# Performance work log

Measured on AMD Instinct MI355X. Metric: run time of the kernel, lower is better.

The kernel has to match this reference:

```python
import jax, jax.numpy as jnp
import numpy as np

N_NODES = 100000


def gcn_conv(x, W, b, src, dst, n_nodes):
    """PyG GCNConv: add self-loops, symmetric normalization, linear, scatter-add, bias."""
    xw = x @ W  # [N, out]
    loop = jnp.arange(n_nodes, dtype=src.dtype)
    src2 = jnp.concatenate([src, loop])  # sources (x_j gathered from here)
    dst2 = jnp.concatenate([dst, loop])  # targets (aggregation index)
    # degree (incl. self-loops) computed at target nodes, unit edge weights
    deg = jax.ops.segment_sum(jnp.ones_like(dst2, dtype=xw.dtype), dst2, num_segments=n_nodes)
    dinv = jnp.where(deg > 0, jax.lax.rsqrt(deg), 0.0)
    norm = dinv[src2] * dinv[dst2]  # [E+N]
    msg = xw[src2] * norm[:, None]  # [E+N, out]  (memory-bound gather)
    out = jax.ops.segment_sum(msg, dst2, num_segments=n_nodes)  # scatter-add
    return out + b


def setup_inputs() -> dict:
    key = jax.random.key(0)
    k1, k2, k3, k4 = jax.random.split(key, 4)
    F_IN, H, C = 128, 128, 64
    E = 1600000
    x = jax.random.normal(k1, (N_NODES, F_IN), dtype=jnp.float32)
    edge_index = jax.random.randint(k2, (2, E), 0, N_NODES, dtype=jnp.int64)
    # Glorot init like PyG GCNConv
    s1 = float(np.sqrt(6.0 / (F_IN + H)))
    s2 = float(np.sqrt(6.0 / (H + C)))
    W1 = jax.random.uniform(k3, (F_IN, H), jnp.float32, -s1, s1)
    W2 = jax.random.uniform(k4, (H, C), jnp.float32, -s2, s2)
    b1 = jnp.zeros((H,), jnp.float32)
    b2 = jnp.zeros((C,), jnp.float32)
    return {"x": x, "edge_index": edge_index, "W1": W1, "b1": b1, "W2": W2, "b2": b2}


def reference(x, edge_index, W1, b1, W2, b2):
    src, dst = edge_index[0], edge_index[1]
    h = gcn_conv(x, W1, b1, src, dst, N_NODES)
    h = jax.nn.relu(h)  # dropout p=0.0 -> identity
    h = gcn_conv(h, W2, b2, src, dst, N_NODES)
    return jax.nn.log_softmax(h, axis=1)
```

## Files before the change

kernel.cpp:

```cpp
#include <hip/hip_runtime.h>
#include <cmath>


#define THREADS 256
#define BSHIFT 8
#define MAXB 512

__device__ __forceinline__ unsigned short f2bf(float f) {
    union { float f; unsigned u; } v; v.f = f;
    unsigned r = v.u + 0x7FFFu + ((v.u >> 16) & 1u);
    return (unsigned short)(r >> 16);
}
__device__ __forceinline__ float bf_lo(unsigned u) {
    union { unsigned u; float f; } v; v.u = u << 16; return v.f;
}
__device__ __forceinline__ float bf_hi(unsigned u) {
    union { unsigned u; float f; } v; v.u = u & 0xFFFF0000u; return v.f;
}

__global__ __launch_bounds__(256) void k_bcount(const int* __restrict__ dst, int E, int B,
                                                int* __restrict__ bcnt) {
    __shared__ int lc[MAXB];
    for (int i = threadIdx.x; i < MAXB; i += 256) lc[i] = 0;
    __syncthreads();
    for (int e = blockIdx.x * blockDim.x + threadIdx.x; e < E; e += gridDim.x * blockDim.x)
        atomicAdd(&lc[dst[e] >> BSHIFT], 1);
    __syncthreads();
    for (int b = threadIdx.x; b < B; b += 256)
        if (lc[b]) atomicAdd(&bcnt[b], lc[b]);
}

__global__ void k_bscan(const int* __restrict__ bcnt, int B, int* __restrict__ boff) {
    __shared__ int sh[MAXB];
    const int t = threadIdx.x;
    int v = (t < B) ? bcnt[t] : 0;
    sh[t] = v; __syncthreads();
    for (int o = 1; o < MAXB; o <<= 1) {
        int add = (t >= o) ? sh[t - o] : 0;
        __syncthreads();
        sh[t] += add;
        __syncthreads();
    }
    if (t < B) boff[t] = sh[t] - v;
    if (t == B - 1) boff[B] = sh[t];
}

__global__ __launch_bounds__(256) void k_bscatter(const int* __restrict__ src,
                                                  const int* __restrict__ dst, int E, int B,
                                                  const int* __restrict__ boff,
                                                  int* __restrict__ bfill,
                                                  unsigned* __restrict__ pairs) {
    __shared__ int lc[MAXB];
    __shared__ int lbase[MAXB];
    const int tid = threadIdx.x;
    const int e0 = blockIdx.x * 8192;
    for (int i = tid; i < MAXB; i += 256) lc[i] = 0;
    __syncthreads();
#pragma unroll
    for (int k = 0; k < 32; k++) {
        int e = e0 + k * 256 + tid;
        if (e < E) atomicAdd(&lc[dst[e] >> BSHIFT], 1);
    }
    __syncthreads();
    for (int b = tid; b < B; b += 256)
        lbase[b] = lc[b] ? atomicAdd(&bfill[b], lc[b]) : 0;
    __syncthreads();
    for (int i = tid; i < MAXB; i += 256) lc[i] = 0;
    __syncthreads();
#pragma unroll
    for (int k = 0; k < 32; k++) {
        int e = e0 + k * 256 + tid;
        if (e < E) {
            int s = src[e], d = dst[e];
            int b = d >> BSHIFT;
            int r = atomicAdd(&lc[b], 1);
            pairs[(size_t)boff[b] + lbase[b] + r] =
                ((unsigned)(d & 255) << 24) | (unsigned)s;
        }
    }
}

__global__ __launch_bounds__(256) void k_bbuild(const unsigned* __restrict__ pairs,
                                                const int* __restrict__ boff, int N,
                                                int* __restrict__ deg,
                                                float* __restrict__ dinv,
                                                int* __restrict__ rowptr,
                                                int* __restrict__ csr_src) {
    __shared__ int ldeg[256], lex[256], lrank[256];
    const int b = blockIdx.x, tid = threadIdx.x;
    const int node0 = b << BSHIFT;
    const int base = boff[b];
    const int cnt_e = boff[b + 1] - base;
    ldeg[tid] = 0;
    __syncthreads();
    for (int e = tid; e < cnt_e; e += 256)
        atomicAdd(&ldeg[pairs[base + e] >> 24], 1);
    __syncthreads();
    int v = ldeg[tid];
    lex[tid] = v; __syncthreads();
    for (int o = 1; o < 256; o <<= 1) {
        int add = (tid >= o) ? lex[tid - o] : 0;
        __syncthreads();
        lex[tid] += add;
        __syncthreads();
    }
    int excl = lex[tid] - v;
    if (node0 + tid < N) {
        deg[node0 + tid] = v;
        dinv[node0 + tid] = rsqrtf((float)(v + 1));
        rowptr[node0 + tid] = base + excl;
    }
    __syncthreads();
    lex[tid] = excl;
    lrank[tid] = 0;
    __syncthreads();
    for (int e = tid; e < cnt_e; e += 256) {
        unsigned p = pairs[base + e];
        int loc = p >> 24;
        int r = atomicAdd(&lrank[loc], 1);
        csr_src[base + lex[loc] + r] = (int)(p & 0xFFFFFFu);
    }
}

__global__ void k_castW(const float* __restrict__ W1, const float* __restrict__ W2,
                        unsigned short* __restrict__ Wt1, unsigned short* __restrict__ Wt2) {
    int idx = blockIdx.x * blockDim.x + threadIdx.x;
    if (idx < 16384) {
        int n = idx >> 7, k = idx & 127;
        Wt1[idx] = f2bf(W1[k * 128 + n]);
    } else if (idx < 16384 + 8192) {
        int t = idx - 16384;
        int n = t >> 7, k = t & 127;
        Wt2[t] = f2bf(W2[k * 64 + n]);
    }
}

typedef __attribute__((ext_vector_type(8))) short bf16x8;
typedef __attribute__((ext_vector_type(4))) float f32x4;

template <int NC, bool A_BF16>
__global__ __launch_bounds__(256) void k_gemm_mfma(const void* __restrict__ Av,
                                                   const unsigned short* __restrict__ Wt,
                                                   const float* __restrict__ dinv,
                                                   unsigned short* __restrict__ Out, int M) {
    constexpr int KP = 136;
    __shared__ __align__(16) short As[64 * KP];
    __shared__ __align__(16) short Bs[NC * KP];
    const int tid = threadIdx.x;
    const int row0 = blockIdx.x * 64;

    if (A_BF16) {
        const unsigned short* A = (const unsigned short*)Av;
#pragma unroll
        for (int q = 0; q < 4; q++) {
            int f = tid + 256 * q;
            int r = f >> 4, c = (f & 15) * 8;
            uint4 v = make_uint4(0, 0, 0, 0);
            if (row0 + r < M) v = *(const uint4*)&A[(size_t)(row0 + r) * 128 + c];
            *(uint4*)&As[r * KP + c] = v;
        }
    } else {
        const float* A = (const float*)Av;
#pragma unroll
        for (int q = 0; q < 8; q++) {
            int f = tid + 256 * q;
            int r = f >> 5, c = (f & 31) * 4;
            float4 v = make_float4(0.f, 0.f, 0.f, 0.f);
            if (row0 + r < M) v = *(const float4*)&A[(size_t)(row0 + r) * 128 + c];
            ushort4 o;
            o.x = f2bf(v.x); o.y = f2bf(v.y); o.z = f2bf(v.z); o.w = f2bf(v.w);
            *(ushort4*)&As[r * KP + c] = o;
        }
    }
    for (int f = tid; f < NC * 16; f += 256) {
        int n = f >> 4, c = (f & 15) * 8;
        *(uint4*)&Bs[n * KP + c] = *(const uint4*)&Wt[n * 128 + c];
    }
    __syncthreads();

    const int wave = tid >> 6, lane = tid & 63;
    const int m = lane & 15, quad = lane >> 4;
    constexpr int CT = NC / 16;
    f32x4 acc[CT] = {};
    const short* arow = &As[(16 * wave + m) * KP + quad * 8];
    const short* brow = &Bs[m * KP + quad * 8];
#pragma unroll
    for (int k0 = 0; k0 < 128; k0 += 32) {
        bf16x8 a = *(const bf16x8*)&arow[k0];
#pragma unroll
        for (int c = 0; c < CT; c++) {
            bf16x8 b = *(const bf16x8*)&brow[(size_t)c * 16 * KP + k0];
            acc[c] = __builtin_amdgcn_mfma_f32_16x16x32_bf16(a, b, acc[c], 0, 0, 0);
        }
    }

    __syncthreads();
    short* Cs = As;
    const int rbase = 16 * wave + quad * 4;
    float dv[4];
#pragma unroll
    for (int r = 0; r < 4; r++) {
        int gr = row0 + rbase + r;
        dv[r] = dinv[gr < M ? gr : 0];
    }
#pragma unroll
    for (int c = 0; c < CT; c++)
#pragma unroll
        for (int r = 0; r < 4; r++)
            Cs[(rbase + r) * NC + 16 * c + m] = (short)f2bf(acc[c][r] * dv[r]);
    __syncthreads();
    for (int f = tid; f < 64 * NC / 8; f += 256) {
        int r = f / (NC / 8), c = (f % (NC / 8)) * 8;
        if (row0 + r < M)
            *(uint4*)&Out[(size_t)(row0 + r) * NC + c] = *(const uint4*)&Cs[r * NC + c];
    }
}

__global__ __launch_bounds__(256) void k_agg128b(const int* __restrict__ csr_src,
                                                 const int* __restrict__ rowptr,
                                                 const int* __restrict__ cnt,
                                                 const float* __restrict__ dinv,
                                                 const unsigned* __restrict__ xw,
                                                 const float* __restrict__ bias,
                                                 unsigned* __restrict__ h1, int N) {
    const int lane = threadIdx.x & 63;
    const int wid = (blockIdx.x * blockDim.x + threadIdx.x) >> 6;
    const int h = lane >> 5, sl = lane & 31;
    const int i = wid * 2 + h;
    if (i >= N) return;
    const float di = dinv[i];
    uint2 u = *(const uint2*)&xw[(size_t)i * 64 + 2 * sl];
    float a0 = bf_lo(u.x), a1 = bf_hi(u.x);
    float a2 = bf_lo(u.y), a3 = bf_hi(u.y);
    const int start = rowptr[i], cn = cnt[i];
    int j = 0;
    for (; j + 8 <= cn; j += 8) {
        int s[8]; uint2 uu[8];
#pragma unroll
        for (int k = 0; k < 8; k++) s[k] = csr_src[start + j + k];
#pragma unroll
        for (int k = 0; k < 8; k++) uu[k] = *(const uint2*)&xw[(size_t)s[k] * 64 + 2 * sl];
#pragma unroll
        for (int k = 0; k < 8; k++) {
            a0 += bf_lo(uu[k].x); a1 += bf_hi(uu[k].x);
            a2 += bf_lo(uu[k].y); a3 += bf_hi(uu[k].y);
        }
    }
    for (; j + 2 <= cn; j += 2) {
        int s0 = csr_src[start + j], s1 = csr_src[start + j + 1];
        uint2 u0 = *(const uint2*)&xw[(size_t)s0 * 64 + 2 * sl];
        uint2 u1 = *(const uint2*)&xw[(size_t)s1 * 64 + 2 * sl];
        a0 += bf_lo(u0.x) + bf_lo(u1.x); a1 += bf_hi(u0.x) + bf_hi(u1.x);
        a2 += bf_lo(u0.y) + bf_lo(u1.y); a3 += bf_hi(u0.y) + bf_hi(u1.y);
    }
    if (j < cn) {
        int s0 = csr_src[start + j];
        uint2 u0 = *(const uint2*)&xw[(size_t)s0 * 64 + 2 * sl];
        a0 += bf_lo(u0.x); a1 += bf_hi(u0.x);
        a2 += bf_lo(u0.y); a3 += bf_hi(u0.y);
    }
    float4 b = *(const float4*)&bias[4 * sl];
    float r0 = fmaxf(di * a0 + b.x, 0.f);
    float r1 = fmaxf(di * a1 + b.y, 0.f);
    float r2 = fmaxf(di * a2 + b.z, 0.f);
    float r3 = fmaxf(di * a3 + b.w, 0.f);
    uint2 o;
    o.x = (unsigned)f2bf(r0) | ((unsigned)f2bf(r1) << 16);
    o.y = (unsigned)f2bf(r2) | ((unsigned)f2bf(r3) << 16);
    *(uint2*)&h1[(size_t)i * 64 + 2 * sl] = o;
}

__global__ __launch_bounds__(256) void k_agg64b(const int* __restrict__ csr_src,
                                                const int* __restrict__ rowptr,
                                                const int* __restrict__ cnt,
                                                const float* __restrict__ dinv,
                                                const unsigned* __restrict__ xw,
                                                const float* __restrict__ bias,
                                                float* __restrict__ out, int N) {
    const int lane = threadIdx.x & 63;
    const int wid = (blockIdx.x * blockDim.x + threadIdx.x) >> 6;
    const int h = lane >> 5;
    const int q = (lane >> 4) & 1;
    const int sl = lane & 15;
    const int i = wid * 2 + h;
    if (i >= N) return;
    const float di = dinv[i];
    float a0 = 0.f, a1 = 0.f, a2 = 0.f, a3 = 0.f;
    if (q == 0) {
        uint2 u = *(const uint2*)&xw[(size_t)i * 32 + 2 * sl];
        a0 = bf_lo(u.x); a1 = bf_hi(u.x); a2 = bf_lo(u.y); a3 = bf_hi(u.y);
    }
    const int start = rowptr[i], cn = cnt[i];
    int e = q;
    for (; e + 6 < cn; e += 8) {
        int s[4]; uint2 uu[4];
#pragma unroll
        for (int k = 0; k < 4; k++) s[k] = csr_src[start + e + 2 * k];
#pragma unroll
        for (int k = 0; k < 4; k++) uu[k] = *(const uint2*)&xw[(size_t)s[k] * 32 + 2 * sl];
#pragma unroll
        for (int k = 0; k < 4; k++) {
            a0 += bf_lo(uu[k].x); a1 += bf_hi(uu[k].x);
            a2 += bf_lo(uu[k].y); a3 += bf_hi(uu[k].y);
        }
    }
    for (; e < cn; e += 2) {
        int s0 = csr_src[start + e];
        uint2 u0 = *(const uint2*)&xw[(size_t)s0 * 32 + 2 * sl];
        a0 += bf_lo(u0.x); a1 += bf_hi(u0.x);
        a2 += bf_lo(u0.y); a3 += bf_hi(u0.y);
    }
    a0 += __shfl_xor(a0, 16); a1 += __shfl_xor(a1, 16);
    a2 += __shfl_xor(a2, 16); a3 += __shfl_xor(a3, 16);
    float4 b = *(const float4*)&bias[4 * sl];
    float v0 = di * a0 + b.x, v1 = di * a1 + b.y;
    float v2 = di * a2 + b.z, v3 = di * a3 + b.w;
    float m = fmaxf(fmaxf(v0, v1), fmaxf(v2, v3));
#pragma unroll
    for (int o = 8; o > 0; o >>= 1) m = fmaxf(m, __shfl_xor(m, o));
    float s2 = expf(v0 - m) + expf(v1 - m) + expf(v2 - m) + expf(v3 - m);
#pragma unroll
    for (int o = 8; o > 0; o >>= 1) s2 += __shfl_xor(s2, o);
    float ls = m + logf(s2);
    if (q == 0)
        *(float4*)&out[(size_t)i * 64 + 4 * sl] =
            make_float4(v0 - ls, v1 - ls, v2 - ls, v3 - ls);
}

extern "C" void kernel_launch(void* const* d_in, const int* in_sizes, int n_in,
                              void* d_out, int out_size, void* d_ws, size_t ws_size,
                              hipStream_t stream) {
    const float* x  = (const float*)d_in[0];
    const int*   ei = (const int*)d_in[1];
    const float* W1 = (const float*)d_in[2];
    const float* b1 = (const float*)d_in[3];
    const float* W2 = (const float*)d_in[4];
    const float* b2 = (const float*)d_in[5];

    const int N = in_sizes[0] / 128;
    const int E = in_sizes[1] / 2;
    const int* src = ei;
    const int* dst = ei + E;
    const int B = (N + 255) >> BSHIFT;

    char* ws = (char*)d_ws;
    size_t off = 0;
    auto alloc = [&](size_t bytes) {
        void* p = ws + off;
        off += (bytes + 255) & ~(size_t)255;
        return p;
    };
    int*            bcnt    = (int*)alloc(MAXB * 4 * 2);
    int*            bfill   = bcnt + MAXB;
    int*            boff    = (int*)alloc((MAXB + 1) * 4);
    int*            deg     = (int*)alloc((size_t)N * 4);
    float*          dinv    = (float*)alloc((size_t)N * 4);
    int*            rowptr  = (int*)alloc((size_t)N * 4);
    int*            csr_src = (int*)alloc((size_t)E * 4);
    unsigned*       pairs   = (unsigned*)alloc((size_t)E * 4);
    unsigned short* Wt1     = (unsigned short*)alloc(128 * 128 * 2);
    unsigned short* Wt2     = (unsigned short*)alloc(64 * 128 * 2);
    unsigned short* xw1     = (unsigned short*)alloc((size_t)N * 128 * 2);
    unsigned short* h1      = (unsigned short*)alloc((size_t)N * 128 * 2);
    unsigned short* hw2     = xw1;
    float*          out     = (float*)d_out;

    hipMemsetAsync(bcnt, 0, MAXB * 4 * 2, stream);

    k_bcount<<<512, THREADS, 0, stream>>>(dst, E, B, bcnt);
    k_bscan<<<1, MAXB, 0, stream>>>(bcnt, B, boff);
    k_bscatter<<<(E + 8191) / 8192, THREADS, 0, stream>>>(src, dst, E, B, boff, bfill, pairs);
    k_bbuild<<<B, THREADS, 0, stream>>>(pairs, boff, N, deg, dinv, rowptr, csr_src);

    k_castW<<<96, THREADS, 0, stream>>>(W1, W2, Wt1, Wt2);

    const int aggBlocks = (N + 7) / 8;

    k_gemm_mfma<128, false><<<(N + 63) / 64, THREADS, 0, stream>>>(x, Wt1, dinv, xw1, N);
    k_agg128b<<<aggBlocks, THREADS, 0, stream>>>(
        csr_src, rowptr, deg, dinv, (const unsigned*)xw1, b1, (unsigned*)h1, N);

    k_gemm_mfma<64, true><<<(N + 63) / 64, THREADS, 0, stream>>>(h1, Wt2, dinv, hw2, N);
    k_agg64b<<<aggBlocks, THREADS, 0, stream>>>(
        csr_src, rowptr, deg, dinv, (const unsigned*)hw2, b2, out, N);
}
```

Baseline: 292.8 us.

## Pad CSR rows to multiples of eight with zero-row sentinel, prefetch indices

```diff
diff --git a/kernel.cpp b/kernel.cpp
--- a/kernel.cpp
+++ b/kernel.cpp
@@ -5,6 +5,7 @@
 #define THREADS 256
 #define BSHIFT 8
 #define MAXB 512
+#define PADSLACK 1792
 
 __device__ __forceinline__ unsigned short f2bf(float f) {
     union { float f; unsigned u; } v; v.f = f;
@@ -90,6 +91,7 @@
     const int b = blockIdx.x, tid = threadIdx.x;
     const int node0 = b << BSHIFT;
     const int base = boff[b];
+    const int pbase = base + b * PADSLACK;
     const int cnt_e = boff[b + 1] - base;
     ldeg[tid] = 0;
     __syncthreads();
@@ -97,29 +99,32 @@
         atomicAdd(&ldeg[pairs[base + e] >> 24], 1);
     __syncthreads();
     int v = ldeg[tid];
-    lex[tid] = v; __syncthreads();
+    int pd = (v + 7) & ~7;
+    lex[tid] = pd; __syncthreads();
     for (int o = 1; o < 256; o <<= 1) {
         int add = (tid >= o) ? lex[tid - o] : 0;
         __syncthreads();
         lex[tid] += add;
         __syncthreads();
     }
-    int excl = lex[tid] - v;
+    int pexcl = lex[tid] - pd;
     if (node0 + tid < N) {
         deg[node0 + tid] = v;
         dinv[node0 + tid] = rsqrtf((float)(v + 1));
-        rowptr[node0 + tid] = base + excl;
-    }
-    __syncthreads();
-    lex[tid] = excl;
+        rowptr[node0 + tid] = pbase + pexcl;
+    }
+    __syncthreads();
+    lex[tid] = pexcl;
     lrank[tid] = 0;
     __syncthreads();
     for (int e = tid; e < cnt_e; e += 256) {
         unsigned p = pairs[base + e];
         int loc = p >> 24;
         int r = atomicAdd(&lrank[loc], 1);
-        csr_src[base + lex[loc] + r] = (int)(p & 0xFFFFFFu);
-    }
+        csr_src[pbase + lex[loc] + r] = (int)(p & 0xFFFFFFu);
+    }
+    for (int p = v; p < pd; p++)
+        csr_src[pbase + pexcl + p] = N;
 }
 
 __global__ void k_castW(const float* __restrict__ W1, const float* __restrict__ W2,
@@ -142,12 +147,16 @@
 __global__ __launch_bounds__(256) void k_gemm_mfma(const void* __restrict__ Av,
                                                    const unsigned short* __restrict__ Wt,
                                                    const float* __restrict__ dinv,
-                                                   unsigned short* __restrict__ Out, int M) {
+                                                   unsigned short* __restrict__ Out,
+                                                   unsigned short* __restrict__ zrow,
+                                                   int M) {
     constexpr int KP = 136;
     __shared__ __align__(16) short As[64 * KP];
     __shared__ __align__(16) short Bs[NC * KP];
     const int tid = threadIdx.x;
     const int row0 = blockIdx.x * 64;
+
+    if (blockIdx.x == 0 && tid < NC) zrow[tid] = 0;
 
     if (A_BF16) {
         const unsigned short* A = (const unsigned short*)Av;
@@ -232,32 +241,22 @@
     uint2 u = *(const uint2*)&xw[(size_t)i * 64 + 2 * sl];
     float a0 = bf_lo(u.x), a1 = bf_hi(u.x);
     float a2 = bf_lo(u.y), a3 = bf_hi(u.y);
-    const int start = rowptr[i], cn = cnt[i];
-    int j = 0;
-    for (; j + 8 <= cn; j += 8) {
-        int s[8]; uint2 uu[8];
-#pragma unroll
-        for (int k = 0; k < 8; k++) s[k] = csr_src[start + j + k];
+    const int start = rowptr[i];
+    const int pc = (cnt[i] + 7) & ~7;
+    int s[8];
+#pragma unroll
+    for (int k = 0; k < 8; k++) s[k] = csr_src[start + k];
+    for (int j = 0; j < pc; j += 8) {
+        uint2 uu[8];
 #pragma unroll
         for (int k = 0; k < 8; k++) uu[k] = *(const uint2*)&xw[(size_t)s[k] * 64 + 2 * sl];
+#pragma unroll
+        for (int k = 0; k < 8; k++) s[k] = csr_src[start + j + 8 + k];
 #pragma unroll
         for (int k = 0; k < 8; k++) {
             a0 += bf_lo(uu[k].x); a1 += bf_hi(uu[k].x);
             a2 += bf_lo(uu[k].y); a3 += bf_hi(uu[k].y);
         }
-    }
-    for (; j + 2 <= cn; j += 2) {
-        int s0 = csr_src[start + j], s1 = csr_src[start + j + 1];
-        uint2 u0 = *(const uint2*)&xw[(size_t)s0 * 64 + 2 * sl];
-        uint2 u1 = *(const uint2*)&xw[(size_t)s1 * 64 + 2 * sl];
-        a0 += bf_lo(u0.x) + bf_lo(u1.x); a1 += bf_hi(u0.x) + bf_hi(u1.x);
-        a2 += bf_lo(u0.y) + bf_lo(u1.y); a3 += bf_hi(u0.y) + bf_hi(u1.y);
-    }
-    if (j < cn) {
-        int s0 = csr_src[start + j];
-        uint2 u0 = *(const uint2*)&xw[(size_t)s0 * 64 + 2 * sl];
-        a0 += bf_lo(u0.x); a1 += bf_hi(u0.x);
-        a2 += bf_lo(u0.y); a3 += bf_hi(u0.y);
     }
     float4 b = *(const float4*)&bias[4 * sl];
     float r0 = fmaxf(di * a0 + b.x, 0.f);
@@ -290,25 +289,22 @@
         uint2 u = *(const uint2*)&xw[(size_t)i * 32 + 2 * sl];
         a0 = bf_lo(u.x); a1 = bf_hi(u.x); a2 = bf_lo(u.y); a3 = bf_hi(u.y);
     }
-    const int start = rowptr[i], cn = cnt[i];
-    int e = q;
-    for (; e + 6 < cn; e += 8) {
-        int s[4]; uint2 uu[4];
-#pragma unroll
-        for (int k = 0; k < 4; k++) s[k] = csr_src[start + e + 2 * k];
+    const int start = rowptr[i];
+    const int pc = (cnt[i] + 7) & ~7;
+    int s[4];
+#pragma unroll
+    for (int k = 0; k < 4; k++) s[k] = csr_src[start + q + 2 * k];
+    for (int e = 0; e < pc; e += 8) {
+        uint2 uu[4];
 #pragma unroll
         for (int k = 0; k < 4; k++) uu[k] = *(const uint2*)&xw[(size_t)s[k] * 32 + 2 * sl];
+#pragma unroll
+        for (int k = 0; k < 4; k++) s[k] = csr_src[start + e + 8 + q + 2 * k];
 #pragma unroll
         for (int k = 0; k < 4; k++) {
             a0 += bf_lo(uu[k].x); a1 += bf_hi(uu[k].x);
             a2 += bf_lo(uu[k].y); a3 += bf_hi(uu[k].y);
         }
-    }
-    for (; e < cn; e += 2) {
-        int s0 = csr_src[start + e];
-        uint2 u0 = *(const uint2*)&xw[(size_t)s0 * 32 + 2 * sl];
-        a0 += bf_lo(u0.x); a1 += bf_hi(u0.x);
-        a2 += bf_lo(u0.y); a3 += bf_hi(u0.y);
     }
     a0 += __shfl_xor(a0, 16); a1 += __shfl_xor(a1, 16);
     a2 += __shfl_xor(a2, 16); a3 += __shfl_xor(a3, 16);
@@ -356,11 +352,11 @@
     int*            deg     = (int*)alloc((size_t)N * 4);
     float*          dinv    = (float*)alloc((size_t)N * 4);
     int*            rowptr  = (int*)alloc((size_t)N * 4);
-    int*            csr_src = (int*)alloc((size_t)E * 4);
+    int*            csr_src = (int*)alloc(((size_t)E + (size_t)B * PADSLACK + 64) * 4);
     unsigned*       pairs   = (unsigned*)alloc((size_t)E * 4);
     unsigned short* Wt1     = (unsigned short*)alloc(128 * 128 * 2);
     unsigned short* Wt2     = (unsigned short*)alloc(64 * 128 * 2);
-    unsigned short* xw1     = (unsigned short*)alloc((size_t)N * 128 * 2);
+    unsigned short* xw1     = (unsigned short*)alloc((size_t)(N + 1) * 128 * 2);
     unsigned short* h1      = (unsigned short*)alloc((size_t)N * 128 * 2);
     unsigned short* hw2     = xw1;
     float*          out     = (float*)d_out;
@@ -376,11 +372,13 @@
 
     const int aggBlocks = (N + 7) / 8;
 
-    k_gemm_mfma<128, false><<<(N + 63) / 64, THREADS, 0, stream>>>(x, Wt1, dinv, xw1, N);
+    k_gemm_mfma<128, false><<<(N + 63) / 64, THREADS, 0, stream>>>(
+        x, Wt1, dinv, xw1, xw1 + (size_t)N * 128, N);
     k_agg128b<<<aggBlocks, THREADS, 0, stream>>>(
         csr_src, rowptr, deg, dinv, (const unsigned*)xw1, b1, (unsigned*)h1, N);
 
-    k_gemm_mfma<64, true><<<(N + 63) / 64, THREADS, 0, stream>>>(h1, Wt2, dinv, hw2, N);
+    k_gemm_mfma<64, true><<<(N + 63) / 64, THREADS, 0, stream>>>(
+        h1, Wt2, dinv, hw2, hw2 + (size_t)N * 64, N);
     k_agg64b<<<aggBlocks, THREADS, 0, stream>>>(
         csr_src, rowptr, deg, dinv, (const unsigned*)hw2, b2, out, N);
 }
```

New measurement: 287.3 us. No clear change (-1.9%).
